# Optimization experiments

Measured on AMD Instinct MI355X. Metric: run time of the kernel, lower is better.

Reference implementation:

```python
import jax, jax.numpy as jnp
import numpy as np
from jax import lax

EPS = 1e-5  # flax BatchNorm default epsilon

def _conv(x, k, b):
    y = lax.conv_general_dilated(x, k, (1, 1), 'SAME', dimension_numbers=('NHWC', 'HWIO', 'NHWC'))
    return y + b

def _bn(x, s, o, m, v):
    # BatchNorm with use_running_average=True (eval mode)
    return (x - m) * (s / jnp.sqrt(v + EPS)) + o

def _pool(x):
    return lax.reduce_window(x, -jnp.inf, lax.max, (1, 2, 2, 1), (1, 2, 2, 1), 'SAME')

def _lstm_last(x_seq, Wi, Wh, b):
    # x_seq: [T,B,D]; Wi: [L,D,4H]; Wh: [L,H,4H]; b: [L,4H].
    # Faithful to original bug: every layer consumes the SAME raw input x_seq
    # (layers are not stacked); only the last layer's hidden states are used.
    B = x_seq.shape[1]
    H = Wh.shape[1]
    def run_layer(Wi_l, Wh_l, b_l):
        def step(carry, xt):
            h, c = carry
            z = xt @ Wi_l + h @ Wh_l + b_l  # [B,4H]
            i, f, g, o = jnp.split(z, 4, axis=-1)
            c2 = jax.nn.sigmoid(f) * c + jax.nn.sigmoid(i) * jnp.tanh(g)
            h2 = jax.nn.sigmoid(o) * jnp.tanh(c2)
            return (h2, c2), h2
        init = (jnp.zeros((B, H), x_seq.dtype), jnp.zeros((B, H), x_seq.dtype))
        _, hs = lax.scan(step, init, x_seq)
        return hs  # [T,B,H]
    hs_all = jax.vmap(run_layer)(Wi, Wh, b)  # [L,T,B,H]
    return hs_all[-1]


def setup_inputs():
    key = jax.random.key(0)
    ks = iter(jax.random.split(key, 64))
    def nrm(shape, scale=0.05):
        return jax.random.normal(next(ks), shape, jnp.float32) * scale
    d = {}
    d['x'] = jax.random.normal(next(ks), (64, 32, 256, 1), jnp.float32)
    cin = [1, 64, 128, 256, 256]
    cout = [64, 128, 256, 256, 512]
    for i in range(5):
        d[f'k{i+1}'] = nrm((3, 3, cin[i], cout[i]))
        d[f'b{i+1}'] = nrm((cout[i],))
        d[f's{i+1}'] = 1.0 + nrm((cout[i],), 0.1)
        d[f'o{i+1}'] = nrm((cout[i],), 0.1)
        d[f'm{i+1}'] = jnp.zeros((cout[i],), jnp.float32)
        d[f'v{i+1}'] = jnp.ones((cout[i],), jnp.float32)
    L, D, H = 2, 2048, 512
    for pre in ('fw', 'bw'):
        d[f'{pre}_Wi'] = nrm((L, D, 4 * H), 0.02)
        d[f'{pre}_Wh'] = nrm((L, H, 4 * H), 0.02)
        d[f'{pre}_b'] = nrm((L, 4 * H), 0.02)
    d['fc_W'] = nrm((2 * H, 80), 0.02)
    d['fc_b'] = nrm((80,), 0.02)
    return d


def reference(x, k1, b1, k2, b2, k3, b3, k4, b4, k5, b5,
              s1, o1, m1, v1, s2, o2, m2, v2, s3, o3, m3, v3,
              s4, o4, m4, v4, s5, o5, m5, v5,
              fw_Wi, fw_Wh, fw_b, bw_Wi, bw_Wh, bw_b, fc_W, fc_b):
    # CNN stem (eval mode: dropout is identity, BN uses running stats)
    x = _pool(_bn(jax.nn.relu(_conv(x, k1, b1)), s1, o1, m1, v1))
    x = _pool(_bn(jax.nn.relu(_conv(x, k2, b2)), s2, o2, m2, v2))
    x = _pool(_bn(jax.nn.relu(_conv(x, k3, b3)), s3, o3, m3, v3))
    x = _bn(jax.nn.relu(_conv(x, k4, b4)), s4, o4, m4, v4)
    x = _bn(jax.nn.relu(_conv(x, k5, b5)), s5, o5, m5, v5)
    b, h, w, c = x.shape
    x = x.reshape(b, w, h * c)        # faithful raw reshape (no transpose), as in original
    x_seq = jnp.swapaxes(x, 0, 1)     # [T,B,D]
    fw = _lstm_last(x_seq, fw_Wi, fw_Wh, fw_b)          # [T,B,H]
    bw = _lstm_last(x_seq[::-1], bw_Wi, bw_Wh, bw_b)    # [T,B,H]; NOT re-flipped (matches original)
    out = jnp.swapaxes(jnp.concatenate([fw, bw], axis=-1), 0, 1)  # [B,T,2H]
    logits = out @ fc_W + fc_b
    return jax.nn.log_softmax(logits, axis=-1)
```

## Files before the change

kernel.cpp:

```cpp
#include <hip/hip_runtime.h>
#include <hip/hip_bf16.h>
#include <math.h>

#define EPSBN 1e-5f

using short8 = __attribute__((ext_vector_type(8))) short;
using f32x4  = __attribute__((ext_vector_type(4))) float;
using us4    = __attribute__((ext_vector_type(4))) unsigned short;

#define MFMA16(a, b, c) __builtin_amdgcn_mfma_f32_16x16x32_bf16(a, b, c, 0, 0, 0)

__device__ __forceinline__ float bf2f(unsigned short u) {
  unsigned int v = ((unsigned int)u) << 16;
  float f;
  __builtin_memcpy(&f, &v, 4);
  return f;
}
__device__ __forceinline__ unsigned short f2bf(float f) {
  __hip_bfloat16 h = __float2bfloat16(f);
  unsigned short u;
  __builtin_memcpy(&u, &h, 2);
  return u;
}
__device__ __forceinline__ float fast_sigmoid(float z) {
  return __builtin_amdgcn_rcpf(1.f + __expf(-z));
}
__device__ __forceinline__ float fast_tanh(float z) {
  float x2 = fminf(fmaxf(2.f * z, -30.f), 30.f);
  float e = __expf(x2);
  return (e - 1.f) * __builtin_amdgcn_rcpf(e + 1.f);
}
__device__ __forceinline__ void stage16(const unsigned short* g, unsigned short* l) {
  __builtin_amdgcn_global_load_lds(
      (const __attribute__((address_space(1))) void*)g,
      (__attribute__((address_space(3))) void*)l, 16, 0, 0);
}

__global__ __launch_bounds__(256) void conv1_pool(
    const float* __restrict__ in, const float* __restrict__ w,
    const float* __restrict__ bias, const float* __restrict__ sc,
    const float* __restrict__ of, const float* __restrict__ mn,
    const float* __restrict__ vr, unsigned short* __restrict__ out) {
  __shared__ float lds[4][258];
  const int blk = blockIdx.x;
  const int b = blk >> 4, y0 = blk & 15;
  const int tid = threadIdx.x;
  for (int i = tid; i < 4 * 258; i += 256) {
    int row = i / 258, c = i - row * 258;
    int iy = 2 * y0 - 1 + row, xx = c - 1;
    float v = 0.f;
    if ((unsigned)iy < 32u && (unsigned)xx < 256u)
      v = in[((b << 5) + iy) * 256 + xx];
    lds[row][c] = v;
  }
  __syncthreads();
  const int co = tid & 63, xg = tid >> 6;
  float w9[9];
  #pragma unroll
  for (int t = 0; t < 9; ++t) w9[t] = w[t * 64 + co];
  const float scale = sc[co] * rsqrtf(vr[co] + EPSBN);
  const float shift = of[co] - mn[co] * scale;
  const float bs = bias[co];
  unsigned short* op = out + (((long)(b * 18 + y0 + 1) * 130 + xg * 32 + 1) << 6) + co;
  for (int px = 0; px < 32; ++px) {
    const int xp = xg * 32 + px;
    float m = -1e30f;
    #pragma unroll
    for (int dy = 0; dy < 2; ++dy) {
      #pragma unroll
      for (int dx = 0; dx < 2; ++dx) {
        const int x = 2 * xp + dx;
        float acc = bs;
        #pragma unroll
        for (int r = 0; r < 3; ++r)
          #pragma unroll
          for (int cc = 0; cc < 3; ++cc)
            acc = fmaf(lds[dy + r][x + cc], w9[r * 3 + cc], acc);
        float v = fmaxf(acc, 0.f) * scale + shift;
        m = fmaxf(m, v);
      }
    }
    op[(long)px << 6] = f2bf(m);
  }
}

template<int C, int H2, int W2>
__global__ __launch_bounds__(256) void maxpool_pad(
    const unsigned short* __restrict__ in, unsigned short* __restrict__ out) {
  constexpr int W2P = W2 + 2, H2P = H2 + 2;
  const int y = blockIdx.y;
  const int b = y / H2P, yp = y - b * H2P;
  const int j = blockIdx.x * 256 + threadIdx.x;
  if (j >= W2P * C) return;
  const int xp = j / C, c = j - xp * C;
  unsigned short res = 0;
  if (yp >= 1 && yp <= H2 && xp >= 1 && xp <= W2) {
    const long rs = (long)(2 * W2) * C;
    const unsigned short* p0 =
        in + (((long)b * (2 * H2) + (yp - 1) * 2) * (2 * W2) + (xp - 1) * 2) * C + c;
    unsigned short u0 = p0[0], u1 = p0[C], u2 = p0[rs], u3 = p0[rs + C];
    unsigned short a = (bf2f(u0) >= bf2f(u1)) ? u0 : u1;
    unsigned short bmx = (bf2f(u2) >= bf2f(u3)) ? u2 : u3;
    res = (bf2f(a) >= bf2f(bmx)) ? a : bmx;
  }
  out[((long)y * W2P + xp) * C + c] = res;
}

struct TAll {
  const float* src[8];
  unsigned short* dst[8];
  int K[8];
  int N[8];
};
__global__ __launch_bounds__(256) void transpose_multi(TAll P) {
  const int z = blockIdx.z;
  const int K = P.K[z], N = P.N[z];
  const int k0 = blockIdx.x * 32, n0 = blockIdx.y * 32;
  if (k0 >= K || n0 >= N) return;
  __shared__ float T[32][33];
  const float* in = P.src[z];
  unsigned short* out = P.dst[z];
  const int tid = threadIdx.x;
  const int r = tid >> 3, c4 = (tid & 7) * 4;
  float4 v = *(const float4*)(in + (long)(k0 + r) * N + n0 + c4);
  T[r][c4 + 0] = v.x; T[r][c4 + 1] = v.y; T[r][c4 + 2] = v.z; T[r][c4 + 3] = v.w;
  __syncthreads();
  us4 o;
  #pragma unroll
  for (int i = 0; i < 4; ++i) o[i] = f2bf(T[c4 + i][r]);
  *(us4*)(out + (long)(n0 + r) * K + k0 + c4) = o;
}

__global__ __launch_bounds__(256) void transpose_fc(
    const float* __restrict__ W, unsigned short* __restrict__ WT) {
  int i = blockIdx.x * 256 + threadIdx.x;
  if (i < 80 * 1024) {
    int n = i >> 10, k = i & 1023;
    WT[i] = f2bf(W[k * 80 + n]);
  }
}

__global__ __launch_bounds__(256) void zero_multi(
    float* p0, long n0, float* p1, long n1, float* p2, long n2, float* p3, long n3) {
  const long i0 = (long)blockIdx.x * 256 + threadIdx.x;
  const long st = (long)gridDim.x * 256;
  for (long j = i0; j < n0; j += st) p0[j] = 0.f;
  for (long j = i0; j < n1; j += st) p1[j] = 0.f;
  for (long j = i0; j < n2; j += st) p2[j] = 0.f;
  for (long j = i0; j < n3; j += st) p3[j] = 0.f;
}

template<int CIN, int COUT, int H, int W, int OUTPAD, int NBM, int NBN>
__global__ __launch_bounds__(256) void conv_mfma128(
    const unsigned short* __restrict__ act, const unsigned short* __restrict__ wT,
    const float* __restrict__ bias, const float* __restrict__ sc,
    const float* __restrict__ of, const float* __restrict__ mn,
    const float* __restrict__ vr, unsigned short* __restrict__ out) {
  constexpr int K9 = 9 * CIN;
  constexpr int HW = H * W;
  constexpr int WP = W + 2;
  constexpr int NK = K9 / 32;
  constexpr int NWG = NBM * NBN;
  constexpr int CSH = (CIN == 64) ? 1 : (CIN == 128) ? 2 : 3;
  constexpr int CMSK = (1 << CSH) - 1;
  __shared__ unsigned short As[2][4096];
  __shared__ unsigned short Bs[2][4096];
  const int tid = threadIdx.x;
  const int lane = tid & 63, wave = tid >> 6;
  const int wzw = blockIdx.x;
  const int logical = (wzw & 7) * (NWG >> 3) + (wzw >> 3);
  const int m0 = (logical % NBM) * 128, n0 = (logical / NBM) * 128;
  const int r0 = tid >> 2, seg = tid & 3;
  const int segp = (seg ^ (r0 & 3)) << 3;
  long pa0, pa1;
  {
    const int m = m0 + r0;
    const int b = m / HW, rem = m % HW;
    const int y = rem / W, x = rem % W;
    pa0 = (((long)b * (H + 2) + y) * WP + x) * CIN + segp;
  }
  {
    const int m = m0 + r0 + 64;
    const int b = m / HW, rem = m % HW;
    const int y = rem / W, x = rem % W;
    pa1 = (((long)b * (H + 2) + y) * WP + x) * CIN + segp;
  }
  const long pb0 = (long)(n0 + r0) * K9 + segp;
  const long pb1 = (long)(n0 + r0 + 64) * K9 + segp;
  const int swz = ((lane >> 4) ^ (lane & 3)) << 3;
  const int arow0 = (wave >> 1) * 64 + (lane & 15);
  const int brow0 = (wave & 1) * 64 + (lane & 15);
  f32x4 acc[4][4] = {};

  auto stage_tile = [&](int ks, int buf) {
    const int tap = ks >> CSH;
    const int cib = (ks & CMSK) << 5;
    const int ty = (tap * 86) >> 8;
    const int tx = tap - ty * 3;
    const long ka = (long)(ty * WP + tx) * CIN + cib;
    const long kb = (long)ks << 5;
    unsigned short* aw = &As[buf][wave * 512];
    unsigned short* bw = &Bs[buf][wave * 512];
    stage16(act + pa0 + ka, aw);
    stage16(act + pa1 + ka, aw + 2048);
    stage16(wT + pb0 + kb, bw);
    stage16(wT + pb1 + kb, bw + 2048);
  };

  stage_tile(0, 0);
  #pragma unroll 1
  for (int ks = 0; ks < NK; ++ks) {
    const int buf = ks & 1;
    if (ks + 1 < NK) {
      stage_tile(ks + 1, buf ^ 1);
      asm volatile("s_waitcnt vmcnt(4)" ::: "memory");
    } else {
      asm volatile("s_waitcnt vmcnt(0)" ::: "memory");
    }
    __builtin_amdgcn_s_barrier();
    __builtin_amdgcn_sched_barrier(0);
    short8 a[4], b[4];
    #pragma unroll
    for (int i = 0; i < 4; ++i)
      a[i] = *(const short8*)(&As[buf][(arow0 + i * 16) * 32 + swz]);
    #pragma unroll
    for (int j = 0; j < 4; ++j)
      b[j] = *(const short8*)(&Bs[buf][(brow0 + j * 16) * 32 + swz]);
    #pragma unroll
    for (int i = 0; i < 4; ++i)
      #pragma unroll
      for (int j = 0; j < 4; ++j)
        acc[i][j] = MFMA16(a[i], b[j], acc[i][j]);
    __builtin_amdgcn_s_barrier();
    __builtin_amdgcn_sched_barrier(0);
  }

  float scl[4], shf[4], bsv[4];
  #pragma unroll
  for (int j = 0; j < 4; ++j) {
    const int col = n0 + (wave & 1) * 64 + j * 16 + (lane & 15);
    scl[j] = sc[col] * rsqrtf(vr[col] + EPSBN);
    shf[j] = of[col] - mn[col] * scl[j];
    bsv[j] = bias[col];
  }
  #pragma unroll
  for (int i = 0; i < 4; ++i) {
    #pragma unroll
    for (int rr = 0; rr < 4; ++rr) {
      const int m = m0 + (wave >> 1) * 64 + i * 16 + (lane >> 4) * 4 + rr;
      const int b = m / HW, rem = m % HW;
      const int y = rem / W, x = rem % W;
      long obase;
      if (OUTPAD) obase = (((long)b * (H + 2) + y + 1) * WP + x + 1) * COUT;
      else        obase = (((long)b * H + y) * W + x) * COUT;
      const int colb = n0 + (wave & 1) * 64 + (lane & 15);
      #pragma unroll
      for (int j = 0; j < 4; ++j) {
        const float v = fmaxf(acc[i][j][rr] + bsv[j], 0.f) * scl[j] + shf[j];
        out[obase + colb + j * 16] = f2bf(v);
      }
    }
  }
}

__global__ __launch_bounds__(256) void gemm_xw2(
    const unsigned short* __restrict__ src,
    const unsigned short* __restrict__ WiTF, const unsigned short* __restrict__ WiTB,
    const float* __restrict__ bF, const float* __restrict__ bB,
    float* __restrict__ xwFp, float* __restrict__ xwBp) {
  __shared__ unsigned short As[2][4096];
  __shared__ unsigned short Bs[2][4096];
  const int rev = blockIdx.z;
  const unsigned short* WiT = rev ? WiTB : WiTF;
  const float* bvec = rev ? bB : bF;
  float* xw = rev ? xwBp : xwFp;
  const int tid = threadIdx.x;
  const int lane = tid & 63, wave = tid >> 6;
  const int wzw = blockIdx.x;
  const int logical = (wzw & 7) * 32 + (wzw >> 3);
  const int m0 = (logical & 15) * 128, n0 = (logical >> 4) * 128;
  const int r0 = tid >> 2, seg = tid & 3;
  const int segp = (seg ^ (r0 & 3)) << 3;
  long pa0, pa1;
  {
    const int r = m0 + r0;
    const int t = r >> 6, bb = r & 63;
    const int tt = rev ? 31 - t : t;
    pa0 = (long)bb * 65536 + (long)tt * 2048 + segp;
  }
  {
    const int r = m0 + r0 + 64;
    const int t = r >> 6, bb = r & 63;
    const int tt = rev ? 31 - t : t;
    pa1 = (long)bb * 65536 + (long)tt * 2048 + segp;
  }
  const long pb0 = (long)(n0 + r0) * 2048 + segp;
  const long pb1 = (long)(n0 + r0 + 64) * 2048 + segp;
  const int swz = ((lane >> 4) ^ (lane & 3)) << 3;
  const int arow0 = (wave >> 1) * 64 + (lane & 15);
  const int brow0 = (wave & 1) * 64 + (lane & 15);
  f32x4 acc[4][4] = {};

  auto stage_tile = [&](int ks, int buf) {
    const long k0 = (long)ks << 5;
    unsigned short* aw = &As[buf][wave * 512];
    unsigned short* bw = &Bs[buf][wave * 512];
    stage16(src + pa0 + k0, aw);
    stage16(src + pa1 + k0, aw + 2048);
    stage16(WiT + pb0 + k0, bw);
    stage16(WiT + pb1 + k0, bw + 2048);
  };

  stage_tile(0, 0);
  #pragma unroll 1
  for (int ks = 0; ks < 64; ++ks) {
    const int buf = ks & 1;
    if (ks + 1 < 64) {
      stage_tile(ks + 1, buf ^ 1);
      asm volatile("s_waitcnt vmcnt(4)" ::: "memory");
    } else {
      asm volatile("s_waitcnt vmcnt(0)" ::: "memory");
    }
    __builtin_amdgcn_s_barrier();
    __builtin_amdgcn_sched_barrier(0);
    short8 a[4], b[4];
    #pragma unroll
    for (int i = 0; i < 4; ++i)
      a[i] = *(const short8*)(&As[buf][(arow0 + i * 16) * 32 + swz]);
    #pragma unroll
    for (int j = 0; j < 4; ++j)
      b[j] = *(const short8*)(&Bs[buf][(brow0 + j * 16) * 32 + swz]);
    #pragma unroll
    for (int i = 0; i < 4; ++i)
      #pragma unroll
      for (int j = 0; j < 4; ++j)
        acc[i][j] = MFMA16(a[i], b[j], acc[i][j]);
    __builtin_amdgcn_s_barrier();
    __builtin_amdgcn_sched_barrier(0);
  }

  float bsv[4];
  #pragma unroll
  for (int j = 0; j < 4; ++j)
    bsv[j] = bvec[n0 + (wave & 1) * 64 + j * 16 + (lane & 15)];
  #pragma unroll
  for (int i = 0; i < 4; ++i) {
    #pragma unroll
    for (int rr = 0; rr < 4; ++rr) {
      const int row = m0 + (wave >> 1) * 64 + i * 16 + (lane >> 4) * 4 + rr;
      const int colb = n0 + (wave & 1) * 64 + (lane & 15);
      #pragma unroll
      for (int j = 0; j < 4; ++j)
        xw[(long)row * 2048 + colb + j * 16] = acc[i][j][rr] + bsv[j];
    }
  }
}

__global__ __launch_bounds__(256) void lstm_persist(
    const unsigned short* __restrict__ WhTF, const unsigned short* __restrict__ WhTB,
    const float* __restrict__ xwF, const float* __restrict__ xwB,
    unsigned short* __restrict__ hsF, unsigned short* __restrict__ hsB,
    int* __restrict__ bar) {
  __shared__ unsigned short Whs[64 * 512];
  __shared__ unsigned short Hs[64 * 512];
  __shared__ float Zs[4 * 64 * 16];
  const int bid = blockIdx.x;
  const int dir = bid >> 5;
  const int nb = bid & 31;
  const int u0 = nb * 16;
  const unsigned short* WhT = dir ? WhTB : WhTF;
  const float* xw = dir ? xwB : xwF;
  unsigned short* hs = dir ? hsB : hsF;
  int* flagbase = bar + dir * 32 * 16;
  int* myflag = flagbase + nb * 16;
  const int tid = threadIdx.x;
  const int lane = tid & 63, wave = tid >> 6;
  const int lr = lane & 15, lk = lane >> 4;
  const int mp = wave >> 1, gp = wave & 1;

  #pragma unroll
  for (int i = 0; i < 16; ++i) {
    const int G = i * 256 + tid;
    const int row = G >> 6, g8 = G & 63;
    const int g = row >> 4, u = row & 15;
    short8 v = *(const short8*)(WhT + ((long)(g * 512 + u0 + u) << 9) + g8 * 8);
    *(short8*)(Whs + row * 512 + ((g8 ^ (row & 7)) << 3)) = v;
  }

  const int prow = tid >> 2;
  const int pu4 = (tid & 3) * 4;
  float c4[4] = {0.f, 0.f, 0.f, 0.f};
  float4 xq[4];
  #pragma unroll
  for (int g = 0; g < 4; ++g)
    xq[g] = *(const float4*)(xw + (long)prow * 2048 + g * 512 + u0 + pu4);

  for (int t = 0; t < 32; ++t) {
    const unsigned short* hsrc = hs + (long)t * 32768;
    #pragma unroll
    for (int i = 0; i < 16; ++i) {
      const int G = i * 256 + tid;
      const int row = G >> 6, g8 = G & 63;
      short8 v = *(const short8*)(hsrc + G * 8);
      *(short8*)(Hs + row * 512 + ((g8 ^ (row & 7)) << 3)) = v;
    }
    __syncthreads();

    f32x4 acc[2][2] = {};
    #pragma unroll
    for (int kk = 0; kk < 16; ++kk) {
      const int sw = ((lk + kk * 4) ^ (lr & 7)) << 3;
      short8 a0 = *(const short8*)(Hs + (mp * 32 + lr) * 512 + sw);
      short8 a1 = *(const short8*)(Hs + (mp * 32 + 16 + lr) * 512 + sw);
      short8 b0 = *(const short8*)(Whs + (gp * 32 + lr) * 512 + sw);
      short8 b1 = *(const short8*)(Whs + (gp * 32 + 16 + lr) * 512 + sw);
      acc[0][0] = MFMA16(a0, b0, acc[0][0]);
      acc[0][1] = MFMA16(a0, b1, acc[0][1]);
      acc[1][0] = MFMA16(a1, b0, acc[1][0]);
      acc[1][1] = MFMA16(a1, b1, acc[1][1]);
    }

    #pragma unroll
    for (int im = 0; im < 2; ++im) {
      const int rowb = (mp * 2 + im) * 16 + lk * 4;
      #pragma unroll
      for (int ig = 0; ig < 2; ++ig) {
        const int g = gp * 2 + ig;
        #pragma unroll
        for (int r = 0; r < 4; ++r)
          Zs[g * 1024 + (rowb + r) * 16 + lr] = acc[im][ig][r];
      }
    }
    __syncthreads();

    {
      float4 zi = *(const float4*)(Zs + tid * 4);
      float4 zf = *(const float4*)(Zs + 1024 + tid * 4);
      float4 zg = *(const float4*)(Zs + 2048 + tid * 4);
      float4 zo = *(const float4*)(Zs + 3072 + tid * 4);
      const float* pzi = (const float*)&zi;
      const float* pzf = (const float*)&zf;
      const float* pzg = (const float*)&zg;
      const float* pzo = (const float*)&zo;
      us4 hv;
      #pragma unroll
      for (int r = 0; r < 4; ++r) {
        float ii = fast_sigmoid(pzi[r] + ((const float*)&xq[0])[r]);
        float ff = fast_sigmoid(pzf[r] + ((const float*)&xq[1])[r]);
        float gg = fast_tanh(pzg[r] + ((const float*)&xq[2])[r]);
        float oo = fast_sigmoid(pzo[r] + ((const float*)&xq[3])[r]);
        c4[r] = ff * c4[r] + ii * gg;
        hv[r] = f2bf(oo * fast_tanh(c4[r]));
      }
      *(us4*)(hs + (long)(t + 1) * 32768 + prow * 512 + u0 + pu4) = hv;
    }

    if (t < 31) {
      float4 xqn[4];
      #pragma unroll
      for (int g = 0; g < 4; ++g)
        xqn[g] = *(const float4*)(xw + (long)((t + 1) * 64 + prow) * 2048 + g * 512 + u0 + pu4);
      __syncthreads();
      if (tid < 64) {
        if (tid == 0)
          __hip_atomic_store(myflag, t + 1, __ATOMIC_RELEASE, __HIP_MEMORY_SCOPE_AGENT);
        int v;
        do {
          v = __hip_atomic_load(flagbase + (tid & 31) * 16,
                                __ATOMIC_ACQUIRE, __HIP_MEMORY_SCOPE_AGENT);
        } while (__any(v < t + 1));
      }
      __syncthreads();
      #pragma unroll
      for (int g = 0; g < 4; ++g) xq[g] = xqn[g];
    }
  }
}

__global__ __launch_bounds__(256) void fc_mfma_ls(
    const unsigned short* __restrict__ hsF, const unsigned short* __restrict__ hsB,
    const unsigned short* __restrict__ WT, const float* __restrict__ bias,
    float* __restrict__ out) {
  __shared__ unsigned short As_[128 * 32];
  __shared__ unsigned short Bs_[80 * 32];
  __shared__ float zbuf[128][81];
  __shared__ float rmax[128];
  __shared__ float rlse[128];
  const int tid = threadIdx.x;
  const int lane = tid & 63, wave = tid >> 6;
  const int m0 = blockIdx.x * 128;
  const int r0 = tid >> 2, seg = tid & 3;
  const int segp = (seg ^ (r0 & 3)) << 3;
  const int swz = ((lane >> 4) ^ (lane & 3)) << 3;
  f32x4 acc[2][5] = {};

  int bA0, tA0, bA1, tA1;
  { int r = m0 + r0;      bA0 = r >> 5; tA0 = r & 31; }
  { int r = m0 + r0 + 64; bA1 = r >> 5; tA1 = r & 31; }

  #pragma unroll 1
  for (int k0 = 0; k0 < 1024; k0 += 32) {
    const unsigned short* src = (k0 < 512) ? hsF : hsB;
    const int koff = k0 & 511;
    stage16(src + (long)(tA0 + 1) * 32768 + bA0 * 512 + koff + segp, As_ + wave * 512);
    stage16(src + (long)(tA1 + 1) * 32768 + bA1 * 512 + koff + segp, As_ + wave * 512 + 2048);
    {
      int G = tid;
      #pragma unroll
      for (int it = 0; it < 2; ++it, G += 256) {
        int rn = G >> 2, sg = G & 3;
        if (rn < 80) {
          short8 v = *(const short8*)(WT + (long)rn * 1024 + k0 + sg * 8);
          *(short8*)(Bs_ + rn * 32 + ((sg ^ (rn & 3)) << 3)) = v;
        }
      }
    }
    __syncthreads();
    short8 a[2], bfrag[5];
    #pragma unroll
    for (int i = 0; i < 2; ++i)
      a[i] = *(const short8*)(As_ + (wave * 32 + i * 16 + (lane & 15)) * 32 + swz);
    #pragma unroll
    for (int j = 0; j < 5; ++j)
      bfrag[j] = *(const short8*)(Bs_ + (j * 16 + (lane & 15)) * 32 + swz);
    #pragma unroll
    for (int i = 0; i < 2; ++i)
      #pragma unroll
      for (int j = 0; j < 5; ++j)
        acc[i][j] = MFMA16(a[i], bfrag[j], acc[i][j]);
    __syncthreads();
  }

  float bsv[5];
  #pragma unroll
  for (int j = 0; j < 5; ++j) bsv[j] = bias[j * 16 + (lane & 15)];
  #pragma unroll
  for (int i = 0; i < 2; ++i)
    #pragma unroll
    for (int j = 0; j < 5; ++j)
      #pragma unroll
      for (int rr = 0; rr < 4; ++rr)
        zbuf[wave * 32 + i * 16 + (lane >> 4) * 4 + rr][j * 16 + (lane & 15)] =
            acc[i][j][rr] + bsv[j];
  __syncthreads();

  if (tid < 128) {
    float mx = -1e30f;
    for (int j = 0; j < 80; ++j) mx = fmaxf(mx, zbuf[tid][j]);
    float s = 0.f;
    for (int j = 0; j < 80; ++j) s += __expf(zbuf[tid][j] - mx);
    rmax[tid] = mx;
    rlse[tid] = logf(s);
  }
  __syncthreads();

  for (int idx = tid; idx < 128 * 80; idx += 256) {
    const int row = idx / 80, j = idx - row * 80;
    out[(long)m0 * 80 + idx] = zbuf[row][j] - rmax[row] - rlse[row];
  }
}

extern "C" void kernel_launch(void* const* d_in, const int* in_sizes, int n_in,
                              void* d_out, int out_size, void* d_ws, size_t ws_size,
                              hipStream_t stream) {
  const float* x  = (const float*)d_in[0];
  const float* k1 = (const float*)d_in[1];  const float* b1 = (const float*)d_in[2];
  const float* s1 = (const float*)d_in[3];  const float* o1 = (const float*)d_in[4];
  const float* m1 = (const float*)d_in[5];  const float* v1 = (const float*)d_in[6];
  const float* k2 = (const float*)d_in[7];  const float* b2 = (const float*)d_in[8];
  const float* s2 = (const float*)d_in[9];  const float* o2 = (const float*)d_in[10];
  const float* m2 = (const float*)d_in[11]; const float* v2 = (const float*)d_in[12];
  const float* k3 = (const float*)d_in[13]; const float* b3 = (const float*)d_in[14];
  const float* s3 = (const float*)d_in[15]; const float* o3 = (const float*)d_in[16];
  const float* m3 = (const float*)d_in[17]; const float* v3 = (const float*)d_in[18];
  const float* k4 = (const float*)d_in[19]; const float* b4 = (const float*)d_in[20];
  const float* s4 = (const float*)d_in[21]; const float* o4 = (const float*)d_in[22];
  const float* m4 = (const float*)d_in[23]; const float* v4 = (const float*)d_in[24];
  const float* k5 = (const float*)d_in[25]; const float* b5 = (const float*)d_in[26];
  const float* s5 = (const float*)d_in[27]; const float* o5 = (const float*)d_in[28];
  const float* m5 = (const float*)d_in[29]; const float* v5 = (const float*)d_in[30];
  const float* fwWi = (const float*)d_in[31];
  const float* fwWh = (const float*)d_in[32];
  const float* fwb  = (const float*)d_in[33];
  const float* bwWi = (const float*)d_in[34];
  const float* bwWh = (const float*)d_in[35];
  const float* bwb  = (const float*)d_in[36];
  const float* fcW  = (const float*)d_in[37];
  const float* fcb  = (const float*)d_in[38];

  char* wsb = (char*)d_ws;
  unsigned short* REG_A = (unsigned short*)(wsb);
  unsigned short* REG_P = (unsigned short*)(wsb + 33554432);
  unsigned short* C4    = (unsigned short*)(wsb + 52723712);
  unsigned short* wT2   = (unsigned short*)(wsb + 59408384);
  unsigned short* wT3   = (unsigned short*)(wsb + 59555840);
  unsigned short* wT4   = (unsigned short*)(wsb + 60145664);
  unsigned short* wT5   = (unsigned short*)(wsb + 61325312);
  unsigned short* WiTF  = (unsigned short*)(wsb + 63684608);
  unsigned short* WiTB  = (unsigned short*)(wsb + 72073216);
  unsigned short* WhTF  = (unsigned short*)(wsb + 80461824);
  unsigned short* WhTB  = (unsigned short*)(wsb + 82558976);
  unsigned short* WTfc  = (unsigned short*)(wsb + 84656128);
  float* xwF = (float*)(wsb + 84819968);
  float* xwB = (float*)(wsb + 101597184);
  int*   bar = (int*)(wsb + 118374400);
  unsigned short* hsF = (unsigned short*)(wsb + 118378496);
  unsigned short* hsB = (unsigned short*)(wsb + 120541184);

  zero_multi<<<2048, 256, 0, stream>>>(
      (float*)(wsb + 118374400), 17408,
      (float*)(wsb + 120541184), 16384,
      (float*)(wsb + 52723712), 1671168,
      (float*)(wsb + 33554432), 4792320);

  TAll tp;
  tp.src[0] = k2; tp.dst[0] = wT2; tp.K[0] = 576;  tp.N[0] = 128;
  tp.src[1] = k3; tp.dst[1] = wT3; tp.K[1] = 1152; tp.N[1] = 256;
  tp.src[2] = k4; tp.dst[2] = wT4; tp.K[2] = 2304; tp.N[2] = 256;
  tp.src[3] = k5; tp.dst[3] = wT5; tp.K[3] = 2304; tp.N[3] = 512;
  tp.src[4] = fwWi + 4194304; tp.dst[4] = WiTF; tp.K[4] = 2048; tp.N[4] = 2048;
  tp.src[5] = bwWi + 4194304; tp.dst[5] = WiTB; tp.K[5] = 2048; tp.N[5] = 2048;
  tp.src[6] = fwWh + 1048576; tp.dst[6] = WhTF; tp.K[6] = 512;  tp.N[6] = 2048;
  tp.src[7] = bwWh + 1048576; tp.dst[7] = WhTB; tp.K[7] = 512;  tp.N[7] = 2048;
  transpose_multi<<<dim3(72, 64, 8), 256, 0, stream>>>(tp);
  transpose_fc<<<320, 256, 0, stream>>>(fcW, WTfc);

  conv1_pool<<<1024, 256, 0, stream>>>(x, k1, b1, s1, o1, m1, v1, REG_P);

  conv_mfma128<64, 128, 16, 128, 0, 1024, 1><<<1024, 256, 0, stream>>>(
      REG_P, wT2, b2, s2, o2, m2, v2, REG_A);
  maxpool_pad<128, 8, 64><<<dim3(33, 640), 256, 0, stream>>>(REG_A, REG_P);

  conv_mfma128<128, 256, 8, 64, 0, 256, 2><<<512, 256, 0, stream>>>(
      REG_P, wT3, b3, s3, o3, m3, v3, REG_A);
  maxpool_pad<256, 4, 32><<<dim3(34, 384), 256, 0, stream>>>(REG_A, REG_P);

  conv_mfma128<256, 256, 4, 32, 1, 64, 2><<<128, 256, 0, stream>>>(
      REG_P, wT4, b4, s4, o4, m4, v4, C4);

  conv_mfma128<256, 512, 4, 32, 0, 64, 4><<<256, 256, 0, stream>>>(
      C4, wT5, b5, s5, o5, m5, v5, REG_A);

  gemm_xw2<<<dim3(256, 1, 2), 256, 0, stream>>>(
      REG_A, WiTF, WiTB, fwb + 2048, bwb + 2048, xwF, xwB);

  lstm_persist<<<64, 256, 0, stream>>>(WhTF, WhTB, xwF, xwB, hsF, hsB, bar);

  fc_mfma_ls<<<16, 256, 0, stream>>>(hsF, hsB, WTfc, fcb, (float*)d_out);
}
```

Baseline: 469.9 us.

## Vectorize maxpool and conv1 stores, merge fc transpose, relax LSTM flag polling

Replaces the scalar maxpool with a version that handles eight bf16 channels per thread using 16-byte loads and stores. conv1 now stages its pooled output row in LDS and writes it with wide coalesced stores. The separate fc weight transpose is folded into the multi-transpose launch as a ninth slice with bounds checks, saving a launch. The LSTM spin-wait uses relaxed loads followed by a single acquire fence, cutting the cost of each poll. These trade a little extra LDS and bounds-check logic for fewer memory transactions and less launch and synchronization overhead.

```diff
diff --git a/kernel.cpp b/kernel.cpp
--- a/kernel.cpp
+++ b/kernel.cpp
@@ -42,6 +42,7 @@
     const float* __restrict__ of, const float* __restrict__ mn,
     const float* __restrict__ vr, unsigned short* __restrict__ out) {
   __shared__ float lds[4][258];
+  __shared__ unsigned short obuf[128 * 64];
   const int blk = blockIdx.x;
   const int b = blk >> 4, y0 = blk & 15;
   const int tid = threadIdx.x;
@@ -61,7 +62,6 @@
   const float scale = sc[co] * rsqrtf(vr[co] + EPSBN);
   const float shift = of[co] - mn[co] * scale;
   const float bs = bias[co];
-  unsigned short* op = out + (((long)(b * 18 + y0 + 1) * 130 + xg * 32 + 1) << 6) + co;
   for (int px = 0; px < 32; ++px) {
     const int xp = xg * 32 + px;
     float m = -1e30f;
@@ -80,37 +80,56 @@
         m = fmaxf(m, v);
       }
     }
-    op[(long)px << 6] = f2bf(m);
-  }
+    obuf[xp * 64 + co] = f2bf(m);
+  }
+  __syncthreads();
+  unsigned short* orow = out + (((long)(b * 18 + y0 + 1) * 130 + 1) << 6);
+  for (int i = tid; i < 1024; i += 256)
+    *(short8*)(orow + i * 8) = *(const short8*)(obuf + i * 8);
 }
 
 template<int C, int H2, int W2>
-__global__ __launch_bounds__(256) void maxpool_pad(
+__global__ __launch_bounds__(256) void maxpool_pad_vec(
     const unsigned short* __restrict__ in, unsigned short* __restrict__ out) {
-  constexpr int W2P = W2 + 2, H2P = H2 + 2;
-  const int y = blockIdx.y;
-  const int b = y / H2P, yp = y - b * H2P;
-  const int j = blockIdx.x * 256 + threadIdx.x;
-  if (j >= W2P * C) return;
-  const int xp = j / C, c = j - xp * C;
-  unsigned short res = 0;
+  constexpr int W2P = W2 + 2, H2P = H2 + 2, C8 = C / 8;
+  const long total = (long)64 * H2P * W2P * C8;
+  long i = (long)blockIdx.x * 256 + threadIdx.x;
+  if (i >= total) return;
+  const int c8 = (int)(i % C8);
+  long r = i / C8;
+  const int xp = (int)(r % W2P); r /= W2P;
+  const int yp = (int)(r % H2P);
+  const int b = (int)(r / H2P);
+  short8 res = {};
   if (yp >= 1 && yp <= H2 && xp >= 1 && xp <= W2) {
     const long rs = (long)(2 * W2) * C;
     const unsigned short* p0 =
-        in + (((long)b * (2 * H2) + (yp - 1) * 2) * (2 * W2) + (xp - 1) * 2) * C + c;
-    unsigned short u0 = p0[0], u1 = p0[C], u2 = p0[rs], u3 = p0[rs + C];
-    unsigned short a = (bf2f(u0) >= bf2f(u1)) ? u0 : u1;
-    unsigned short bmx = (bf2f(u2) >= bf2f(u3)) ? u2 : u3;
-    res = (bf2f(a) >= bf2f(bmx)) ? a : bmx;
-  }
-  out[((long)y * W2P + xp) * C + c] = res;
+        in + (((long)b * (2 * H2) + (yp - 1) * 2) * (2 * W2) + (xp - 1) * 2) * C + c8 * 8;
+    short8 v00 = *(const short8*)(p0);
+    short8 v01 = *(const short8*)(p0 + C);
+    short8 v10 = *(const short8*)(p0 + rs);
+    short8 v11 = *(const short8*)(p0 + rs + C);
+    #pragma unroll
+    for (int e = 0; e < 8; ++e) {
+      float f0 = bf2f((unsigned short)v00[e]), f1 = bf2f((unsigned short)v01[e]);
+      float f2 = bf2f((unsigned short)v10[e]), f3 = bf2f((unsigned short)v11[e]);
+      float mx = fmaxf(fmaxf(f0, f1), fmaxf(f2, f3));
+      unsigned short uu;
+      if (mx == f0) uu = (unsigned short)v00[e];
+      else if (mx == f1) uu = (unsigned short)v01[e];
+      else if (mx == f2) uu = (unsigned short)v10[e];
+      else uu = (unsigned short)v11[e];
+      res[e] = (short)uu;
+    }
+  }
+  *(short8*)(out + (((long)b * H2P + yp) * W2P + xp) * C + c8 * 8) = res;
 }
 
 struct TAll {
-  const float* src[8];
-  unsigned short* dst[8];
-  int K[8];
-  int N[8];
+  const float* src[9];
+  unsigned short* dst[9];
+  int K[9];
+  int N[9];
 };
 __global__ __launch_bounds__(256) void transpose_multi(TAll P) {
   const int z = blockIdx.z;
@@ -122,21 +141,22 @@
   unsigned short* out = P.dst[z];
   const int tid = threadIdx.x;
   const int r = tid >> 3, c4 = (tid & 7) * 4;
-  float4 v = *(const float4*)(in + (long)(k0 + r) * N + n0 + c4);
-  T[r][c4 + 0] = v.x; T[r][c4 + 1] = v.y; T[r][c4 + 2] = v.z; T[r][c4 + 3] = v.w;
+  if (n0 + 32 <= N) {
+    float4 v = *(const float4*)(in + (long)(k0 + r) * N + n0 + c4);
+    T[r][c4 + 0] = v.x; T[r][c4 + 1] = v.y; T[r][c4 + 2] = v.z; T[r][c4 + 3] = v.w;
+  } else {
+    #pragma unroll
+    for (int i = 0; i < 4; ++i) {
+      int col = n0 + c4 + i;
+      T[r][c4 + i] = (col < N) ? in[(long)(k0 + r) * N + col] : 0.f;
+    }
+  }
   __syncthreads();
-  us4 o;
-  #pragma unroll
-  for (int i = 0; i < 4; ++i) o[i] = f2bf(T[c4 + i][r]);
-  *(us4*)(out + (long)(n0 + r) * K + k0 + c4) = o;
-}
-
-__global__ __launch_bounds__(256) void transpose_fc(
-    const float* __restrict__ W, unsigned short* __restrict__ WT) {
-  int i = blockIdx.x * 256 + threadIdx.x;
-  if (i < 80 * 1024) {
-    int n = i >> 10, k = i & 1023;
-    WT[i] = f2bf(W[k * 80 + n]);
+  if (n0 + r < N) {
+    us4 o;
+    #pragma unroll
+    for (int i = 0; i < 4; ++i) o[i] = f2bf(T[c4 + i][r]);
+    *(us4*)(out + (long)(n0 + r) * K + k0 + c4) = o;
   }
 }
 
@@ -467,10 +487,11 @@
         int v;
         do {
           v = __hip_atomic_load(flagbase + (tid & 31) * 16,
-                                __ATOMIC_ACQUIRE, __HIP_MEMORY_SCOPE_AGENT);
+                                __ATOMIC_RELAXED, __HIP_MEMORY_SCOPE_AGENT);
         } while (__any(v < t + 1));
       }
       __syncthreads();
+      __builtin_amdgcn_fence(__ATOMIC_ACQUIRE, "agent");
       #pragma unroll
       for (int g = 0; g < 4; ++g) xq[g] = xqn[g];
     }
@@ -622,18 +643,18 @@
   tp.src[5] = bwWi + 4194304; tp.dst[5] = WiTB; tp.K[5] = 2048; tp.N[5] = 2048;
   tp.src[6] = fwWh + 1048576; tp.dst[6] = WhTF; tp.K[6] = 512;  tp.N[6] = 2048;
   tp.src[7] = bwWh + 1048576; tp.dst[7] = WhTB; tp.K[7] = 512;  tp.N[7] = 2048;
-  transpose_multi<<<dim3(72, 64, 8), 256, 0, stream>>>(tp);
-  transpose_fc<<<320, 256, 0, stream>>>(fcW, WTfc);
+  tp.src[8] = fcW; tp.dst[8] = WTfc; tp.K[8] = 1024; tp.N[8] = 80;
+  transpose_multi<<<dim3(72, 64, 9), 256, 0, stream>>>(tp);
 
   conv1_pool<<<1024, 256, 0, stream>>>(x, k1, b1, s1, o1, m1, v1, REG_P);
 
   conv_mfma128<64, 128, 16, 128, 0, 1024, 1><<<1024, 256, 0, stream>>>(
       REG_P, wT2, b2, s2, o2, m2, v2, REG_A);
-  maxpool_pad<128, 8, 64><<<dim3(33, 640), 256, 0, stream>>>(REG_A, REG_P);
+  maxpool_pad_vec<128, 8, 64><<<2640, 256, 0, stream>>>(REG_A, REG_P);
 
   conv_mfma128<128, 256, 8, 64, 0, 256, 2><<<512, 256, 0, stream>>>(
       REG_P, wT3, b3, s3, o3, m3, v3, REG_A);
-  maxpool_pad<256, 4, 32><<<dim3(34, 384), 256, 0, stream>>>(REG_A, REG_P);
+  maxpool_pad_vec<256, 4, 32><<<1632, 256, 0, stream>>>(REG_A, REG_P);
 
   conv_mfma128<256, 256, 4, 32, 1, 64, 2><<<128, 256, 0, stream>>>(
       REG_P, wT4, b4, s4, o4, m4, v4, C4);
```

After: 487.2 us. 3.7% more time.
